# Kernel optimization log

Measured on AMD Instinct MI355X. Metric: run time of the kernel, lower is better.

## Reference

```python
import jax, jax.numpy as jnp
import numpy as np

FACTOR = 5  # init factor


def setup_inputs() -> dict:
    key = jax.random.key(0)
    k1, k2, k3, k4 = jax.random.split(key, 4)
    B, H, L, D = 4, 8, 2048, 64
    sample_k = min(FACTOR * int(np.ceil(np.log(L))), L)  # 40
    queries = jax.random.normal(k1, (B, H, L, D), dtype=jnp.float32)
    keys = jax.random.normal(k2, (B, H, L, D), dtype=jnp.float32)
    values = jax.random.normal(k3, (B, H, L, D), dtype=jnp.float32)
    index_sample = jax.random.randint(k4, (L, sample_k), 0, L)
    return {"queries": queries, "keys": keys, "values": values,
            "index_sample": index_sample}


def reference(queries, keys, values, index_sample):
    B, H, L_Q, D = queries.shape
    L_K = keys.shape[2]
    n_top = min(FACTOR * int(np.ceil(np.log(L_Q))), L_Q)

    # --- _prob_QK ---
    # Gather sampled keys per query position: [B,H,L_Q,sample_k,D]
    K_sample = keys[:, :, index_sample, :]
    # Q.unsqueeze(3) @ K_sample^T -> [B,H,L_Q,sample_k]
    Q_K_sample = jnp.einsum('bhld,bhlsd->bhls', queries, K_sample)
    # sparsity measure M = max - mean
    M = Q_K_sample.max(axis=-1) - Q_K_sample.sum(axis=-1) / L_K
    _, M_top = jax.lax.top_k(M, n_top)  # [B,H,n_top]
    # gather top queries: [B,H,n_top,D]
    Q_reduce = jnp.take_along_axis(queries, M_top[..., None], axis=2)
    # full scores for top queries: [B,H,n_top,L_K]
    scores_top = jnp.einsum('bhud,bhkd->bhuk', Q_reduce, keys)

    # --- scale ---
    scale = 1.0 / np.sqrt(D).astype(np.float32)
    scores_top = scores_top * scale

    # --- initial context (mask_flag=False): mean of V broadcast over L_Q ---
    V_mean = values.mean(axis=2)  # [B,H,D]
    context = jnp.broadcast_to(V_mean[:, :, None, :], (B, H, L_Q, D))

    # --- update context at top-query positions ---
    attn = jax.nn.softmax(scores_top, axis=-1)           # [B,H,n_top,L_K]
    ctx_update = jnp.einsum('bhuk,bhkd->bhud', attn, values)
    b_idx = jnp.arange(B)[:, None, None]
    h_idx = jnp.arange(H)[None, :, None]
    context = context.at[b_idx, h_idx, M_top].set(ctx_update)
    return context
```

## Files before the change

### kernel.cpp

```cpp
#include <hip/hip_runtime.h>
#include <math.h>

#define BH 32
#define L  2048
#define D  64
#define SK 40
#define NT 40
#define NC 16
#define CK 128
#define SCALE 0.125f

#define WS_M      0
#define WS_MTOP   262144
#define WS_VP     267264
#define WS_VM     332800
#define WS_OPART  344064
#define WS_MPART  5586944
#define WS_LPART  5668864

__global__ __launch_bounds__(256) void kMV(const float* __restrict__ Q,
                                           const float* __restrict__ K,
                                           const float* __restrict__ V,
                                           const int* __restrict__ idx,
                                           float* __restrict__ M,
                                           float* __restrict__ Vp)
{
    __shared__ int   sidx[64 * SK];
    __shared__ float red[256];

    int t = threadIdx.x;
    if (blockIdx.x < 1024) {
        int b    = blockIdx.x;
        int xcd  = b & 7;
        int head = ((b >> 3) & 3) * 8 + xcd;
        int qc   = b >> 5;
        int l0   = qc * 64;

        for (int i = t; i < 64 * SK; i += 256) sidx[i] = idx[l0 * SK + i];
        __syncthreads();

        int wave = t >> 6, lane = t & 63;
        int g  = lane >> 2;
        int dl = lane & 3;
        int lq = wave * 16 + g;
        int l  = l0 + lq;
        int qid = head * L + l;

        const float4* Q4 = reinterpret_cast<const float4*>(Q);
        float4 q0 = Q4[(size_t)qid * 16 + dl * 4 + 0];
        float4 q1 = Q4[(size_t)qid * 16 + dl * 4 + 1];
        float4 q2 = Q4[(size_t)qid * 16 + dl * 4 + 2];
        float4 q3 = Q4[(size_t)qid * 16 + dl * 4 + 3];
        const float4* Kb4 = reinterpret_cast<const float4*>(K) + (size_t)head * L * 16;

        float mx = -INFINITY, sm = 0.f;
        #pragma unroll 4
        for (int s = 0; s < SK; ++s) {
            int kr = sidx[lq * SK + s];
            const float4* kp = Kb4 + (size_t)kr * 16 + dl * 4;
            float4 k0 = kp[0], k1 = kp[1], k2 = kp[2], k3 = kp[3];
            float p = q0.x * k0.x + q0.y * k0.y + q0.z * k0.z + q0.w * k0.w
                    + q1.x * k1.x + q1.y * k1.y + q1.z * k1.z + q1.w * k1.w
                    + q2.x * k2.x + q2.y * k2.y + q2.z * k2.z + q2.w * k2.w
                    + q3.x * k3.x + q3.y * k3.y + q3.z * k3.z + q3.w * k3.w;
            p += __shfl_xor(p, 1, 64);
            p += __shfl_xor(p, 2, 64);
            mx = fmaxf(mx, p);
            sm += p;
        }
        if (dl == 0) M[qid] = mx - sm * (1.0f / (float)L);
    } else {
        int b2 = blockIdx.x - 1024;
        int bh = b2 >> 3, c = b2 & 7;
        int dl = t & 63;
        int gg = t >> 6;
        const float* Vb = V + (size_t)bh * L * D;
        float acc = 0.f;
        int base = c * 256 + gg * 64;
        for (int k = 0; k < 64; ++k) acc += Vb[(size_t)(base + k) * D + dl];
        red[t] = acc;
        __syncthreads();
        if (t < 64)
            Vp[b2 * 64 + dl] = red[dl] + red[64 + dl] + red[128 + dl] + red[192 + dl];
    }
}

__global__ __launch_bounds__(256) void kTopVm(const float* __restrict__ M,
                                              const float* __restrict__ Vp,
                                              int* __restrict__ Mtop,
                                              float* __restrict__ Vm)
{
    __shared__ unsigned int keys[L];
    __shared__ int hist[256];
    __shared__ int ssum[256];
    __shared__ int bsel;
    __shared__ unsigned int pref_s;
    __shared__ int krem_s;
    __shared__ int cnt_gt, cnt_eq;
    __shared__ int eqlist[64];

    int bh = blockIdx.x;
    int t  = threadIdx.x;

    if (t < 64) {
        float s = 0.f;
        #pragma unroll
        for (int c = 0; c < 8; ++c) s += Vp[(bh * 8 + c) * 64 + t];
        Vm[bh * D + t] = s * (1.0f / (float)L);
    }

    for (int i = t; i < L; i += 256) {
        unsigned int u = __float_as_uint(M[bh * L + i]);
        keys[i] = (u & 0x80000000u) ? ~u : (u | 0x80000000u);
    }
    if (t == 0) { pref_s = 0u; krem_s = NT; cnt_gt = 0; cnt_eq = 0; }
    __syncthreads();

    #pragma unroll
    for (int shift = 24; shift >= 0; shift -= 8) {
        hist[t] = 0;
        __syncthreads();
        unsigned int pref = pref_s;
        for (int i = t; i < L; i += 256) {
            unsigned int k  = keys[i];
            unsigned int hi = (shift == 24) ? 0u : (k >> (shift + 8));
            if (hi == pref) atomicAdd(&hist[(k >> shift) & 0xFF], 1);
        }
        __syncthreads();
        ssum[t] = hist[t];
        __syncthreads();
        for (int st = 1; st < 256; st <<= 1) {
            int v = (t + st < 256) ? ssum[t + st] : 0;
            __syncthreads();
            ssum[t] += v;
            __syncthreads();
        }
        int krem = krem_s;
        int excl = ssum[t] - hist[t];
        if (excl < krem && excl + hist[t] >= krem) bsel = t;
        __syncthreads();
        if (t == 0) {
            int bb = bsel;
            krem_s = krem_s - (ssum[bb] - hist[bb]);
            pref_s = (pref_s << 8) | (unsigned int)bb;
        }
        __syncthreads();
    }

    unsigned int T = pref_s;
    int krem = krem_s;
    for (int i = t; i < L; i += 256) {
        unsigned int k = keys[i];
        if (k > T) {
            int p = atomicAdd(&cnt_gt, 1);
            Mtop[bh * NT + p] = i;
        } else if (k == T) {
            int p = atomicAdd(&cnt_eq, 1);
            if (p < 64) eqlist[p] = i;
        }
    }
    __syncthreads();
    if (t == 0) {
        int base = cnt_gt;
        int m = cnt_eq < 64 ? cnt_eq : 64;
        for (int q = 0; q < krem; ++q) {
            int best = 0x7fffffff, bj = -1;
            for (int j = 0; j < m; ++j) if (eqlist[j] < best) { best = eqlist[j]; bj = j; }
            Mtop[bh * NT + base + q] = best;
            if (bj >= 0) eqlist[bj] = 0x7fffffff;
        }
    }
}

__global__ __launch_bounds__(256, 2) void kAttnPart(const float* __restrict__ Q,
                                                    const float* __restrict__ K,
                                                    const float* __restrict__ V,
                                                    const int* __restrict__ Mtop,
                                                    const float* __restrict__ Vm,
                                                    float* __restrict__ Opart,
                                                    float* __restrict__ mpart,
                                                    float* __restrict__ lpart,
                                                    float* __restrict__ out)
{
    __shared__ float4 KV4[CK * 16];
    __shared__ float4 Qs4[NT * 16];
    __shared__ float  S[NT * CK];
    __shared__ int    mrow[NT];
    __shared__ float  smax[NT], ssum[NT];

    int c = blockIdx.x, bh = blockIdx.y;
    int t = threadIdx.x;

    {
        const float4* Vm4 = reinterpret_cast<const float4*>(Vm + bh * D);
        float4* outB = reinterpret_cast<float4*>(out) + ((size_t)bh * L + c * CK) * 16;
        #pragma unroll
        for (int k = 0; k < 8; ++k) { int i = t + k * 256; outB[i] = Vm4[i & 15]; }
    }

    if (t < NT) mrow[t] = Mtop[bh * NT + t];
    __syncthreads();

    const float4* Qg = reinterpret_cast<const float4*>(Q) + (size_t)bh * L * 16;
    for (int i = t; i < NT * 16; i += 256) {
        int u = i >> 4, d4 = i & 15;
        Qs4[i] = Qg[(size_t)mrow[u] * 16 + d4];
    }
    const float4* Kg = reinterpret_cast<const float4*>(K) + ((size_t)bh * L + c * CK) * 16;
    for (int i = t; i < CK * 16; i += 256) {
        int j = i >> 4, d4 = i & 15;
        KV4[j * 16 + (d4 ^ (j & 15))] = Kg[i];
    }
    __syncthreads();

    {
        int wave = t >> 6, lane = t & 63;
        int jh = wave & 1, uh = wave >> 1;
        int j = jh * 64 + lane;
        float4 k4[16];
        #pragma unroll
        for (int d4 = 0; d4 < 16; ++d4) k4[d4] = KV4[j * 16 + (d4 ^ (j & 15))];
        for (int u = uh * 20; u < uh * 20 + 20; ++u) {
            float acc = 0.f;
            #pragma unroll
            for (int d4 = 0; d4 < 16; ++d4) {
                float4 q4 = Qs4[u * 16 + d4];
                acc += k4[d4].x * q4.x + k4[d4].y * q4.y
                     + k4[d4].z * q4.z + k4[d4].w * q4.w;
            }
            S[u * CK + j] = acc * SCALE;
        }
    }
    __syncthreads();

    const float4* Vg = reinterpret_cast<const float4*>(V) + ((size_t)bh * L + c * CK) * 16;
    float4 vreg[8];
    #pragma unroll
    for (int k = 0; k < 8; ++k) vreg[k] = Vg[t + k * 256];

    {
        int wave = t >> 6, lane = t & 63;
        for (int u = wave * 10; u < wave * 10 + 10; ++u) {
            float s0 = S[u * CK + lane], s1 = S[u * CK + 64 + lane];
            float m = fmaxf(s0, s1);
            #pragma unroll
            for (int o = 1; o < 64; o <<= 1) m = fmaxf(m, __shfl_xor(m, o, 64));
            float e0 = __expf(s0 - m), e1 = __expf(s1 - m);
            S[u * CK + lane] = e0; S[u * CK + 64 + lane] = e1;
            float l2 = e0 + e1;
            #pragma unroll
            for (int o = 1; o < 64; o <<= 1) l2 += __shfl_xor(l2, o, 64);
            if (lane == 0) { smax[u] = m; ssum[u] = l2; }
        }
    }
    __syncthreads();

    #pragma unroll
    for (int k = 0; k < 8; ++k) {
        int i = t + k * 256;
        int j = i >> 4, d4 = i & 15;
        KV4[j * 16 + (d4 ^ (j & 15))] = vreg[k];
    }
    __syncthreads();

    {
        int a = t >> 5, r = t & 31;
        int d4 = r >> 1, jh = r & 1;
        float4 acc[5];
        #pragma unroll
        for (int ui = 0; ui < 5; ++ui) acc[ui] = make_float4(0.f, 0.f, 0.f, 0.f);
        for (int jj = 0; jj < 64; ++jj) {
            int j = jh * 64 + jj;
            float4 v4 = KV4[j * 16 + (d4 ^ (j & 15))];
            #pragma unroll
            for (int ui = 0; ui < 5; ++ui) {
                float p = S[(a + 8 * ui) * CK + j];
                acc[ui].x += p * v4.x; acc[ui].y += p * v4.y;
                acc[ui].z += p * v4.z; acc[ui].w += p * v4.w;
            }
        }
        #pragma unroll
        for (int ui = 0; ui < 5; ++ui) {
            acc[ui].x += __shfl_xor(acc[ui].x, 1, 64);
            acc[ui].y += __shfl_xor(acc[ui].y, 1, 64);
            acc[ui].z += __shfl_xor(acc[ui].z, 1, 64);
            acc[ui].w += __shfl_xor(acc[ui].w, 1, 64);
        }
        if (jh == 0) {
            float4* Og = reinterpret_cast<float4*>(Opart) + ((size_t)(bh * NC + c) * NT) * 16;
            #pragma unroll
            for (int ui = 0; ui < 5; ++ui)
                Og[(a + 8 * ui) * 16 + d4] = acc[ui];
        }
    }
    if (t < NT) {
        mpart[(bh * NC + c) * NT + t] = smax[t];
        lpart[(bh * NC + c) * NT + t] = ssum[t];
    }
}

__global__ __launch_bounds__(64) void kCombine(const float* __restrict__ Opart,
                                               const float* __restrict__ mpart,
                                               const float* __restrict__ lpart,
                                               const int* __restrict__ Mtop,
                                               float* __restrict__ out)
{
    int u = blockIdx.x, bh = blockIdx.y, d = threadIdx.x;
    float gm = -INFINITY, den = 0.f, o = 0.f;
    for (int c = 0; c < NC; ++c) {
        int pi = (bh * NC + c) * NT + u;
        float mv = mpart[pi], lv = lpart[pi];
        float nm = fmaxf(gm, mv);
        float r1 = __expf(gm - nm), r2 = __expf(mv - nm);
        o   = o * r1 + r2 * Opart[(size_t)pi * D + d];
        den = den * r1 + r2 * lv;
        gm  = nm;
    }
    int qrow = Mtop[bh * NT + u];
    out[((size_t)bh * L + qrow) * D + d] = o / den;
}

extern "C" void kernel_launch(void* const* d_in, const int* in_sizes, int n_in,
                              void* d_out, int out_size, void* d_ws, size_t ws_size,
                              hipStream_t stream)
{
    const float* Q   = (const float*)d_in[0];
    const float* K   = (const float*)d_in[1];
    const float* V   = (const float*)d_in[2];
    const int*   idx = (const int*)d_in[3];
    float* out = (float*)d_out;

    char* ws = (char*)d_ws;
    float* M     = (float*)(ws + WS_M);
    int*   Mtop  = (int*)  (ws + WS_MTOP);
    float* Vp    = (float*)(ws + WS_VP);
    float* Vm    = (float*)(ws + WS_VM);
    float* Opart = (float*)(ws + WS_OPART);
    float* mpart = (float*)(ws + WS_MPART);
    float* lpart = (float*)(ws + WS_LPART);

    kMV      <<<1280, 256, 0, stream>>>(Q, K, V, idx, M, Vp);
    kTopVm   <<<BH, 256, 0, stream>>>(M, Vp, Mtop, Vm);
    kAttnPart<<<dim3(NC, BH), 256, 0, stream>>>(Q, K, V, Mtop, Vm, Opart, mpart, lpart, out);
    kCombine <<<dim3(NT, BH), 64, 0, stream>>>(Opart, mpart, lpart, Mtop, out);
}
```

Before: 179.7 us.

## Fuse V-mean into sampling kernel, pregather top queries, register-resident QK scores

The sampling kernel now computes the partial V sums in every block instead of in separate tail blocks. It uses 512 threads with 8 lanes per query and DPP reductions in place of shuffles. The top-k kernel also gathers the selected query rows into a Qtop buffer. The attention kernel keeps K rows and scores in registers and fuses the softmax without staging K/Q in shared memory, padding the S stride to avoid bank conflicts and dropping two barriers. The cost is higher register pressure in the attention kernel and more Vp partials to reduce in the top-k kernel.

```diff
diff --git a/kernel.cpp b/kernel.cpp
--- a/kernel.cpp
+++ b/kernel.cpp
@@ -8,17 +8,25 @@
 #define NT 40
 #define NC 16
 #define CK 128
+#define SP 129
 #define SCALE 0.125f
 
 #define WS_M      0
 #define WS_MTOP   262144
 #define WS_VP     267264
-#define WS_VM     332800
-#define WS_OPART  344064
-#define WS_MPART  5586944
-#define WS_LPART  5668864
-
-__global__ __launch_bounds__(256) void kMV(const float* __restrict__ Q,
+#define WS_VM     529408
+#define WS_QTOP   537600
+#define WS_OPART  865280
+#define WS_MPART  6108160
+#define WS_LPART  6190080
+
+template <int CTRL>
+__device__ __forceinline__ float dpp_add(float x) {
+    int y = __builtin_amdgcn_update_dpp(0, __float_as_int(x), CTRL, 0xF, 0xF, true);
+    return x + __int_as_float(y);
+}
+
+__global__ __launch_bounds__(512) void kMV(const float* __restrict__ Q,
                                            const float* __restrict__ K,
                                            const float* __restrict__ V,
                                            const int* __restrict__ idx,
@@ -26,69 +34,65 @@
                                            float* __restrict__ Vp)
 {
     __shared__ int   sidx[64 * SK];
-    __shared__ float red[256];
-
-    int t = threadIdx.x;
-    if (blockIdx.x < 1024) {
-        int b    = blockIdx.x;
-        int xcd  = b & 7;
-        int head = ((b >> 3) & 3) * 8 + xcd;
-        int qc   = b >> 5;
-        int l0   = qc * 64;
-
-        for (int i = t; i < 64 * SK; i += 256) sidx[i] = idx[l0 * SK + i];
-        __syncthreads();
-
-        int wave = t >> 6, lane = t & 63;
-        int g  = lane >> 2;
-        int dl = lane & 3;
-        int lq = wave * 16 + g;
-        int l  = l0 + lq;
-        int qid = head * L + l;
-
-        const float4* Q4 = reinterpret_cast<const float4*>(Q);
-        float4 q0 = Q4[(size_t)qid * 16 + dl * 4 + 0];
-        float4 q1 = Q4[(size_t)qid * 16 + dl * 4 + 1];
-        float4 q2 = Q4[(size_t)qid * 16 + dl * 4 + 2];
-        float4 q3 = Q4[(size_t)qid * 16 + dl * 4 + 3];
-        const float4* Kb4 = reinterpret_cast<const float4*>(K) + (size_t)head * L * 16;
-
-        float mx = -INFINITY, sm = 0.f;
-        #pragma unroll 4
-        for (int s = 0; s < SK; ++s) {
-            int kr = sidx[lq * SK + s];
-            const float4* kp = Kb4 + (size_t)kr * 16 + dl * 4;
-            float4 k0 = kp[0], k1 = kp[1], k2 = kp[2], k3 = kp[3];
-            float p = q0.x * k0.x + q0.y * k0.y + q0.z * k0.z + q0.w * k0.w
-                    + q1.x * k1.x + q1.y * k1.y + q1.z * k1.z + q1.w * k1.w
-                    + q2.x * k2.x + q2.y * k2.y + q2.z * k2.z + q2.w * k2.w
-                    + q3.x * k3.x + q3.y * k3.y + q3.z * k3.z + q3.w * k3.w;
-            p += __shfl_xor(p, 1, 64);
-            p += __shfl_xor(p, 2, 64);
-            mx = fmaxf(mx, p);
-            sm += p;
-        }
-        if (dl == 0) M[qid] = mx - sm * (1.0f / (float)L);
-    } else {
-        int b2 = blockIdx.x - 1024;
-        int bh = b2 >> 3, c = b2 & 7;
-        int dl = t & 63;
-        int gg = t >> 6;
-        const float* Vb = V + (size_t)bh * L * D;
+    __shared__ float red[512];
+
+    int t    = threadIdx.x;
+    int b    = blockIdx.x;
+    int head = ((b >> 3) & 3) * 8 + (b & 7);
+    int qc   = b >> 5;
+    int l0   = qc * 64;
+
+    {
+        int d = t & 63, r = t >> 6;
+        const float* Vb = V + ((size_t)head * L + l0 + r * 8) * D + d;
         float acc = 0.f;
-        int base = c * 256 + gg * 64;
-        for (int k = 0; k < 64; ++k) acc += Vb[(size_t)(base + k) * D + dl];
+        #pragma unroll
+        for (int k = 0; k < 8; ++k) acc += Vb[(size_t)k * D];
         red[t] = acc;
-        __syncthreads();
-        if (t < 64)
-            Vp[b2 * 64 + dl] = red[dl] + red[64 + dl] + red[128 + dl] + red[192 + dl];
-    }
+    }
+    for (int i = t; i < 64 * SK; i += 512) sidx[i] = idx[l0 * SK + i];
+    __syncthreads();
+    if (t < 64) {
+        float s = 0.f;
+        #pragma unroll
+        for (int rr = 0; rr < 8; ++rr) s += red[t + rr * 64];
+        Vp[(head * 32 + qc) * 64 + t] = s;
+    }
+
+    int wave = t >> 6, lane = t & 63;
+    int g  = lane >> 3;
+    int dl = lane & 7;
+    int lq = wave * 8 + g;
+    size_t qid = (size_t)head * L + (l0 + lq);
+
+    const float4* Q4 = reinterpret_cast<const float4*>(Q);
+    float4 q0 = Q4[qid * 16 + dl * 2 + 0];
+    float4 q1 = Q4[qid * 16 + dl * 2 + 1];
+    const float4* Kb4 = reinterpret_cast<const float4*>(K) + (size_t)head * L * 16;
+
+    float mx = -INFINITY, sm = 0.f;
+    #pragma unroll 4
+    for (int s = 0; s < SK; ++s) {
+        int kr = sidx[lq * SK + s];
+        const float4* kp = Kb4 + (size_t)kr * 16 + dl * 2;
+        float4 k0 = kp[0], k1 = kp[1];
+        float p = q0.x * k0.x + q0.y * k0.y + q0.z * k0.z + q0.w * k0.w
+                + q1.x * k1.x + q1.y * k1.y + q1.z * k1.z + q1.w * k1.w;
+        p = dpp_add<0xB1>(p);
+        p = dpp_add<0x4E>(p);
+        p = dpp_add<0x12C>(p);
+        mx = fmaxf(mx, p);
+        sm += p;
+    }
+    if (dl == 0) M[qid] = mx - sm * (1.0f / (float)L);
 }
 
 __global__ __launch_bounds__(256) void kTopVm(const float* __restrict__ M,
                                               const float* __restrict__ Vp,
+                                              const float* __restrict__ Q,
                                               int* __restrict__ Mtop,
-                                              float* __restrict__ Vm)
+                                              float* __restrict__ Vm,
+                                              float* __restrict__ Qtop)
 {
     __shared__ unsigned int keys[L];
     __shared__ int hist[256];
@@ -98,6 +102,7 @@
     __shared__ int krem_s;
     __shared__ int cnt_gt, cnt_eq;
     __shared__ int eqlist[64];
+    __shared__ int stop[NT];
 
     int bh = blockIdx.x;
     int t  = threadIdx.x;
@@ -105,7 +110,7 @@
     if (t < 64) {
         float s = 0.f;
         #pragma unroll
-        for (int c = 0; c < 8; ++c) s += Vp[(bh * 8 + c) * 64 + t];
+        for (int c = 0; c < 32; ++c) s += Vp[(bh * 32 + c) * 64 + t];
         Vm[bh * D + t] = s * (1.0f / (float)L);
     }
 
@@ -154,6 +159,7 @@
         if (k > T) {
             int p = atomicAdd(&cnt_gt, 1);
             Mtop[bh * NT + p] = i;
+            stop[p] = i;
         } else if (k == T) {
             int p = atomicAdd(&cnt_eq, 1);
             if (p < 64) eqlist[p] = i;
@@ -167,25 +173,28 @@
             int best = 0x7fffffff, bj = -1;
             for (int j = 0; j < m; ++j) if (eqlist[j] < best) { best = eqlist[j]; bj = j; }
             Mtop[bh * NT + base + q] = best;
+            stop[base + q] = best;
             if (bj >= 0) eqlist[bj] = 0x7fffffff;
         }
     }
-}
-
-__global__ __launch_bounds__(256, 2) void kAttnPart(const float* __restrict__ Q,
+    __syncthreads();
+    const float4* Qg = reinterpret_cast<const float4*>(Q) + (size_t)bh * L * 16;
+    float4* Qt = reinterpret_cast<float4*>(Qtop) + (size_t)bh * NT * 16;
+    for (int i = t; i < NT * 16; i += 256)
+        Qt[i] = Qg[(size_t)stop[i >> 4] * 16 + (i & 15)];
+}
+
+__global__ __launch_bounds__(256, 2) void kAttnPart(const float* __restrict__ Qtop,
                                                     const float* __restrict__ K,
                                                     const float* __restrict__ V,
-                                                    const int* __restrict__ Mtop,
                                                     const float* __restrict__ Vm,
                                                     float* __restrict__ Opart,
                                                     float* __restrict__ mpart,
                                                     float* __restrict__ lpart,
                                                     float* __restrict__ out)
 {
-    __shared__ float4 KV4[CK * 16];
-    __shared__ float4 Qs4[NT * 16];
-    __shared__ float  S[NT * CK];
-    __shared__ int    mrow[NT];
+    __shared__ float4 V4[CK * 16];
+    __shared__ float  S[NT * SP];
     __shared__ float  smax[NT], ssum[NT];
 
     int c = blockIdx.x, bh = blockIdx.y;
@@ -198,68 +207,56 @@
         for (int k = 0; k < 8; ++k) { int i = t + k * 256; outB[i] = Vm4[i & 15]; }
     }
 
-    if (t < NT) mrow[t] = Mtop[bh * NT + t];
-    __syncthreads();
-
-    const float4* Qg = reinterpret_cast<const float4*>(Q) + (size_t)bh * L * 16;
-    for (int i = t; i < NT * 16; i += 256) {
-        int u = i >> 4, d4 = i & 15;
-        Qs4[i] = Qg[(size_t)mrow[u] * 16 + d4];
-    }
-    const float4* Kg = reinterpret_cast<const float4*>(K) + ((size_t)bh * L + c * CK) * 16;
-    for (int i = t; i < CK * 16; i += 256) {
-        int j = i >> 4, d4 = i & 15;
-        KV4[j * 16 + (d4 ^ (j & 15))] = Kg[i];
-    }
-    __syncthreads();
-
-    {
-        int wave = t >> 6, lane = t & 63;
-        int jh = wave & 1, uh = wave >> 1;
-        int j = jh * 64 + lane;
-        float4 k4[16];
-        #pragma unroll
-        for (int d4 = 0; d4 < 16; ++d4) k4[d4] = KV4[j * 16 + (d4 ^ (j & 15))];
-        for (int u = uh * 20; u < uh * 20 + 20; ++u) {
-            float acc = 0.f;
-            #pragma unroll
-            for (int d4 = 0; d4 < 16; ++d4) {
-                float4 q4 = Qs4[u * 16 + d4];
-                acc += k4[d4].x * q4.x + k4[d4].y * q4.y
-                     + k4[d4].z * q4.z + k4[d4].w * q4.w;
-            }
-            S[u * CK + j] = acc * SCALE;
-        }
-    }
-    __syncthreads();
-
     const float4* Vg = reinterpret_cast<const float4*>(V) + ((size_t)bh * L + c * CK) * 16;
     float4 vreg[8];
     #pragma unroll
     for (int k = 0; k < 8; ++k) vreg[k] = Vg[t + k * 256];
 
-    {
-        int wave = t >> 6, lane = t & 63;
-        for (int u = wave * 10; u < wave * 10 + 10; ++u) {
-            float s0 = S[u * CK + lane], s1 = S[u * CK + 64 + lane];
-            float m = fmaxf(s0, s1);
-            #pragma unroll
-            for (int o = 1; o < 64; o <<= 1) m = fmaxf(m, __shfl_xor(m, o, 64));
-            float e0 = __expf(s0 - m), e1 = __expf(s1 - m);
-            S[u * CK + lane] = e0; S[u * CK + 64 + lane] = e1;
-            float l2 = e0 + e1;
-            #pragma unroll
-            for (int o = 1; o < 64; o <<= 1) l2 += __shfl_xor(l2, o, 64);
-            if (lane == 0) { smax[u] = m; ssum[u] = l2; }
-        }
-    }
-    __syncthreads();
+    int w    = __builtin_amdgcn_readfirstlane(t) >> 6;
+    int lane = t & 63;
+    const float4* Kg = reinterpret_cast<const float4*>(K) + ((size_t)bh * L + c * CK) * 16;
+    float4 k0[16], k1[16];
+    #pragma unroll
+    for (int d4 = 0; d4 < 16; ++d4) {
+        k0[d4] = Kg[(size_t)lane * 16 + d4];
+        k1[d4] = Kg[(size_t)(64 + lane) * 16 + d4];
+    }
+
+    const float* Qb = Qtop + ((size_t)bh * NT + w * 10) * D;
+    float p0[10], p1[10];
+    #pragma unroll
+    for (int i = 0; i < 10; ++i) {
+        const float* qrow = Qb + i * D;
+        float a0 = 0.f, a1 = 0.f;
+        #pragma unroll
+        for (int d4 = 0; d4 < 16; ++d4) {
+            float4 q4 = *reinterpret_cast<const float4*>(qrow + d4 * 4);
+            a0 += q4.x * k0[d4].x + q4.y * k0[d4].y + q4.z * k0[d4].z + q4.w * k0[d4].w;
+            a1 += q4.x * k1[d4].x + q4.y * k1[d4].y + q4.z * k1[d4].z + q4.w * k1[d4].w;
+        }
+        p0[i] = a0 * SCALE; p1[i] = a1 * SCALE;
+    }
+
+    #pragma unroll
+    for (int i = 0; i < 10; ++i) {
+        int u = w * 10 + i;
+        float m = fmaxf(p0[i], p1[i]);
+        #pragma unroll
+        for (int o = 1; o < 64; o <<= 1) m = fmaxf(m, __shfl_xor(m, o, 64));
+        float e0 = __expf(p0[i] - m), e1 = __expf(p1[i] - m);
+        float l2 = e0 + e1;
+        #pragma unroll
+        for (int o = 1; o < 64; o <<= 1) l2 += __shfl_xor(l2, o, 64);
+        S[u * SP + lane]      = e0;
+        S[u * SP + 64 + lane] = e1;
+        if (lane == 0) { smax[u] = m; ssum[u] = l2; }
+    }
 
     #pragma unroll
     for (int k = 0; k < 8; ++k) {
         int i = t + k * 256;
         int j = i >> 4, d4 = i & 15;
-        KV4[j * 16 + (d4 ^ (j & 15))] = vreg[k];
+        V4[j * 16 + (d4 ^ (j & 15))] = vreg[k];
     }
     __syncthreads();
 
@@ -271,20 +268,20 @@
         for (int ui = 0; ui < 5; ++ui) acc[ui] = make_float4(0.f, 0.f, 0.f, 0.f);
         for (int jj = 0; jj < 64; ++jj) {
             int j = jh * 64 + jj;
-            float4 v4 = KV4[j * 16 + (d4 ^ (j & 15))];
+            float4 v4 = V4[j * 16 + (d4 ^ (j & 15))];
             #pragma unroll
             for (int ui = 0; ui < 5; ++ui) {
-                float p = S[(a + 8 * ui) * CK + j];
+                float p = S[(a + 8 * ui) * SP + j];
                 acc[ui].x += p * v4.x; acc[ui].y += p * v4.y;
                 acc[ui].z += p * v4.z; acc[ui].w += p * v4.w;
             }
         }
         #pragma unroll
         for (int ui = 0; ui < 5; ++ui) {
-            acc[ui].x += __shfl_xor(acc[ui].x, 1, 64);
-            acc[ui].y += __shfl_xor(acc[ui].y, 1, 64);
-            acc[ui].z += __shfl_xor(acc[ui].z, 1, 64);
-            acc[ui].w += __shfl_xor(acc[ui].w, 1, 64);
+            acc[ui].x = dpp_add<0xB1>(acc[ui].x);
+            acc[ui].y = dpp_add<0xB1>(acc[ui].y);
+            acc[ui].z = dpp_add<0xB1>(acc[ui].z);
+            acc[ui].w = dpp_add<0xB1>(acc[ui].w);
         }
         if (jh == 0) {
             float4* Og = reinterpret_cast<float4*>(Opart) + ((size_t)(bh * NC + c) * NT) * 16;
@@ -335,12 +332,13 @@
     int*   Mtop  = (int*)  (ws + WS_MTOP);
     float* Vp    = (float*)(ws + WS_VP);
     float* Vm    = (float*)(ws + WS_VM);
+    float* Qtop  = (float*)(ws + WS_QTOP);
     float* Opart = (float*)(ws + WS_OPART);
     float* mpart = (float*)(ws + WS_MPART);
     float* lpart = (float*)(ws + WS_LPART);
 
-    kMV      <<<1280, 256, 0, stream>>>(Q, K, V, idx, M, Vp);
-    kTopVm   <<<BH, 256, 0, stream>>>(M, Vp, Mtop, Vm);
-    kAttnPart<<<dim3(NC, BH), 256, 0, stream>>>(Q, K, V, Mtop, Vm, Opart, mpart, lpart, out);
+    kMV      <<<1024, 512, 0, stream>>>(Q, K, V, idx, M, Vp);
+    kTopVm   <<<BH, 256, 0, stream>>>(M, Vp, Q, Mtop, Vm, Qtop);
+    kAttnPart<<<dim3(NC, BH), 256, 0, stream>>>(Qtop, K, V, Vm, Opart, mpart, lpart, out);
     kCombine <<<dim3(NT, BH), 64, 0, stream>>>(Opart, mpart, lpart, Mtop, out);
 }
```

Result: faster. 165.5 us (-7.9%).
